# Kernel tuning notes

Hardware: AMD Instinct MI355X
Metric: run time of the kernel (lower is better)

The kernel has to match this reference:

```python
import jax, jax.numpy as jnp
import numpy as np

N = 100000   # nodes
E = 1600000  # edges
NC = 10000   # candidates
G = 1000     # graphs
ND = 32      # node_emb_dim
ED = 8       # edge_emb_dim
L = 4        # num_layers


def setup_inputs() -> dict:
    key = jax.random.key(0)
    ks = jax.random.split(key, 12)
    s = 0.1
    return {
        "x": jax.random.normal(ks[0], (N, 2), dtype=jnp.float32),
        "edge_attr": jax.random.normal(ks[1], (E, 1), dtype=jnp.float32),
        "Wn_in": jax.random.normal(ks[2], (2, ND)) * s,
        "bn_in": jnp.zeros((ND,)),
        "We_in": jax.random.normal(ks[3], (1, ED)) * s,
        "be_in": jnp.zeros((ED,)),
        "We_l": jax.random.normal(ks[4], (L, 2 * ND + ED, ED)) * s,
        "be_l": jnp.zeros((L, ED)),
        "Wn_l": jax.random.normal(ks[5], (L, ND + ED, ND)) * s,
        "bn_l": jnp.zeros((L, ND)),
        "Wout": jax.random.normal(ks[6], (ND, 1)) * s,
        "bout": jnp.zeros((1,)),
        "edge_index": jax.random.randint(ks[7], (2, E), 0, N),
        "batch": jnp.sort(jax.random.randint(ks[8], (N,), 0, G)),
        "candidate_idxs": jax.random.randint(ks[9], (NC,), 0, N),
    }


def reference(x, edge_attr, Wn_in, bn_in, We_in, be_in, We_l, be_l, Wn_l, bn_l,
              Wout, bout, edge_index, batch, candidate_idxs):
    h = x @ Wn_in + bn_in            # [N, ND]
    e = edge_attr @ We_in + be_in    # [E, ED]
    src, dst = edge_index[0], edge_index[1]
    for l in range(L):
        # edge update: MLP on [x_src, x_dst, edge_attr]
        m = jnp.concatenate([h[src], h[dst], e], axis=-1)        # [E, 2*ND+ED]
        new_e = jax.nn.relu(m @ We_l[l] + be_l[l])               # [E, ED]
        # aggregate (aggr='add') messages at destination nodes
        agg = jax.ops.segment_sum(new_e, dst, num_segments=N)    # [N, ED]
        new_h = jax.nn.relu(jnp.concatenate([h, agg], axis=-1) @ Wn_l[l] + bn_l[l])
        h = h + new_h   # residual
        e = e + new_e   # residual
    logits = (h[candidate_idxs] @ Wout + bout)[:, 0]             # [NC]
    seg = batch[candidate_idxs]                                  # [NC] graph ids
    # scatter_log_softmax over per-graph candidate groups
    mx = jax.ops.segment_max(logits, seg, num_segments=G)
    shifted = logits - mx[seg]
    lse = jnp.log(jax.ops.segment_sum(jnp.exp(shifted), seg, num_segments=G))
    return shifted - lse[seg]
```

## Files before the change

### kernel.cpp

```cpp
#include <hip/hip_runtime.h>

#define ND 32
#define ED 8
#define NL 4
#define NG 1000
#define NBC_MAX 512
#define CHUNK 8192
#define CHUNK_H 4096
#define NBLK 64

typedef unsigned short u16;

__device__ __forceinline__ int xcd_swizzle(int b, int nb) {
  int per = nb >> 3;
  return (b < (per << 3)) ? ((b & 7) * per + (b >> 3)) : b;
}


__device__ __forceinline__ u16 f2bf(float f) {
  unsigned u = __float_as_uint(f);
  u += 0x7fffu + ((u >> 16) & 1u);
  return (u16)(u >> 16);
}
__device__ __forceinline__ unsigned pack2(float a, float b) {
  return (unsigned)f2bf(a) | ((unsigned)f2bf(b) << 16);
}
__device__ __forceinline__ void cvt8(uint4 p, float* o) {
  o[0] = __uint_as_float(p.x << 16); o[1] = __uint_as_float(p.x & 0xffff0000u);
  o[2] = __uint_as_float(p.y << 16); o[3] = __uint_as_float(p.y & 0xffff0000u);
  o[4] = __uint_as_float(p.z << 16); o[5] = __uint_as_float(p.z & 0xffff0000u);
  o[6] = __uint_as_float(p.w << 16); o[7] = __uint_as_float(p.w & 0xffff0000u);
}
__device__ __forceinline__ uint4 pack8(const float* v) {
  uint4 o;
  o.x = pack2(v[0], v[1]); o.y = pack2(v[2], v[3]);
  o.z = pack2(v[4], v[5]); o.w = pack2(v[6], v[7]);
  return o;
}


__global__ void k_init_h(const float* __restrict__ x,
                         const float* __restrict__ W,
                         const float* __restrict__ b,
                         const float* __restrict__ We,
                         const float* __restrict__ be,
                         u16* __restrict__ h,
                         u16* __restrict__ zs, u16* __restrict__ zd,
                         int N) {
  int n = xcd_swizzle(blockIdx.x, gridDim.x) * blockDim.x + threadIdx.x;
  if (n >= N) return;
  float x0 = x[2 * n], x1 = x[2 * n + 1];
  float v[ND];
#pragma unroll
  for (int d = 0; d < ND; ++d) v[d] = fmaf(x0, W[d], fmaf(x1, W[ND + d], b[d]));
#pragma unroll
  for (int d = 0; d < ND; ++d) v[d] = __uint_as_float((unsigned)f2bf(v[d]) << 16);
  uint4* h4 = reinterpret_cast<uint4*>(h + (size_t)n * ND);
#pragma unroll
  for (int q = 0; q < 4; ++q) h4[q] = pack8(&v[q * 8]);
  float zsv[ED], zdv[ED];
#pragma unroll
  for (int j = 0; j < ED; ++j) { zsv[j] = 0.0f; zdv[j] = be[j]; }
#pragma unroll
  for (int k = 0; k < ND; ++k)
#pragma unroll
    for (int j = 0; j < ED; ++j) {
      zsv[j] = fmaf(v[k], We[k * ED + j], zsv[j]);
      zdv[j] = fmaf(v[k], We[(ND + k) * ED + j], zdv[j]);
    }
  *reinterpret_cast<uint4*>(zs + (size_t)n * ED) = pack8(zsv);
  *reinterpret_cast<uint4*>(zd + (size_t)n * ED) = pack8(zdv);
}


__global__ void k_chist(const int* __restrict__ dst, int* __restrict__ bcnt,
                        int E, int nbc) {
  __shared__ int lcnt[NBC_MAX];
  for (int b = threadIdx.x; b < nbc; b += blockDim.x) lcnt[b] = 0;
  __syncthreads();
  int e0 = blockIdx.x * CHUNK_H;
  int e1 = min(e0 + CHUNK_H, E);
  for (int i = e0 + threadIdx.x; i < e1; i += blockDim.x)
    atomicAdd(&lcnt[dst[i] >> 8], 1);
  __syncthreads();
  for (int b = threadIdx.x; b < nbc; b += blockDim.x)
    if (lcnt[b]) atomicAdd(&bcnt[b], lcnt[b]);
}

__global__ void k_cscan(const int* __restrict__ bcnt, int* __restrict__ bbase,
                        int nbc) {
  __shared__ int s[NBC_MAX];
  int tid = threadIdx.x;
  if (nbc <= NBC_MAX) {
    int v = (tid < nbc) ? bcnt[tid] : 0;
    s[tid] = v;
    __syncthreads();
    for (int st = 1; st < NBC_MAX; st <<= 1) {
      int t = (tid >= st) ? s[tid - st] : 0;
      __syncthreads();
      s[tid] += t;
      __syncthreads();
    }
    if (tid < nbc) bbase[tid] = s[tid] - v;
    if (tid == nbc - 1) bbase[nbc] = s[tid];
  } else if (tid == 0) {
    int run = 0;
    for (int i = 0; i < nbc; ++i) { bbase[i] = run; run += bcnt[i]; }
    bbase[nbc] = run;
  }
}

__global__ void k_binA(const int* __restrict__ src, const int* __restrict__ dst,
                       const float* __restrict__ ea,
                       const int* __restrict__ bbase, int* __restrict__ cursor_c,
                       uint2* __restrict__ binned, int E, int nbc) {
  __shared__ int lcnt[NBC_MAX];
  __shared__ int lbase[NBC_MAX];
  for (int b = threadIdx.x; b < nbc; b += blockDim.x) lcnt[b] = 0;
  __syncthreads();
  int e0 = blockIdx.x * CHUNK;
  int e1 = min(e0 + CHUNK, E);
  for (int i = e0 + threadIdx.x; i < e1; i += blockDim.x)
    atomicAdd(&lcnt[dst[i] >> 8], 1);
  __syncthreads();
  for (int b = threadIdx.x; b < nbc; b += blockDim.x) {
    int c = lcnt[b];
    lbase[b] = c ? (bbase[b] + atomicAdd(&cursor_c[b], c)) : 0;
  }
  __syncthreads();
  for (int i = e0 + threadIdx.x; i < e1; i += blockDim.x) {
    int d = dst[i];
    int pos = atomicAdd(&lbase[d >> 8], 1);
    binned[pos] = make_uint2((unsigned)src[i] | ((unsigned)(d & 255) << 24),
                             __float_as_uint(ea[i]));
  }
}

__global__ void k_binB(const uint2* __restrict__ binned,
                       const int* __restrict__ bbase,
                       uint2* __restrict__ sedge, u16* __restrict__ e,
                       int* __restrict__ noffs,
                       const float* __restrict__ We,
                       const float* __restrict__ be,
                       int N) {
  __shared__ int hist[256];
  __shared__ int scn[256];
  int b = blockIdx.x;
  int base = bbase[b], end = bbase[b + 1];
  int node0 = b << 8;
  int nn = min(256, N - node0);
  hist[threadIdx.x] = 0;
  __syncthreads();
  for (int p = base + threadIdx.x; p < end; p += blockDim.x)
    atomicAdd(&hist[binned[p].x >> 24], 1);
  __syncthreads();
  int v = hist[threadIdx.x];
  scn[threadIdx.x] = v;
  __syncthreads();
  for (int st = 1; st < 256; st <<= 1) {
    int t = (threadIdx.x >= (unsigned)st) ? scn[threadIdx.x - st] : 0;
    __syncthreads();
    scn[threadIdx.x] += t;
    __syncthreads();
  }
  int excl = base + scn[threadIdx.x] - v;
  if ((int)threadIdx.x < nn) noffs[node0 + threadIdx.x] = excl;
  if (threadIdx.x == 0) noffs[min(node0 + 256, N)] = end;
  hist[threadIdx.x] = excl;
  __syncthreads();
  for (int p = base + threadIdx.x; p < end; p += blockDim.x) {
    uint2 rec = binned[p];
    int dl = (int)(rec.x >> 24);
    int pos = atomicAdd(&hist[dl], 1);
    sedge[pos] = make_uint2(rec.x & 0xffffffu, (unsigned)(node0 + dl));
    float a = __uint_as_float(rec.y);
    float e0[ED];
#pragma unroll
    for (int j = 0; j < ED; ++j) e0[j] = fmaf(a, We[j], be[j]);
    *reinterpret_cast<uint4*>(e + (size_t)pos * ED) = pack8(e0);
  }
}


template <bool LAST>
__global__ void k_edge(const u16* __restrict__ zs,
                       const u16* __restrict__ zd,
                       u16* __restrict__ e,
                       u16* __restrict__ ne,
                       const uint2* __restrict__ sedge,
                       const float* __restrict__ W3,
                       int E) {
  int i = xcd_swizzle(blockIdx.x, gridDim.x) * blockDim.x + threadIdx.x;
  if (i >= E) return;
  uint2 sd = sedge[i];
  float zsv[ED], zdv[ED], ein[ED], acc[ED];
  cvt8(*reinterpret_cast<const uint4*>(zs + (size_t)sd.x * ED), zsv);
  cvt8(*reinterpret_cast<const uint4*>(zd + (size_t)sd.y * ED), zdv);
  cvt8(*reinterpret_cast<const uint4*>(e + (size_t)i * ED), ein);
#pragma unroll
  for (int j = 0; j < ED; ++j) acc[j] = zsv[j] + zdv[j];
#pragma unroll
  for (int k = 0; k < ED; ++k)
#pragma unroll
    for (int j = 0; j < ED; ++j)
      acc[j] = fmaf(ein[k], W3[k * ED + j], acc[j]);
#pragma unroll
  for (int j = 0; j < ED; ++j) acc[j] = fmaxf(acc[j], 0.0f);
  *reinterpret_cast<uint4*>(ne + (size_t)i * ED) = pack8(acc);
  if (!LAST) {
    float eo[ED];
#pragma unroll
    for (int j = 0; j < ED; ++j) eo[j] = ein[j] + acc[j];
    *reinterpret_cast<uint4*>(e + (size_t)i * ED) = pack8(eo);
  }
}

template <bool PROJ>
__global__ void k_node(u16* __restrict__ h,
                       const u16* __restrict__ ne,
                       const int* __restrict__ noffs,
                       const float* __restrict__ W,
                       const float* __restrict__ b,
                       const float* __restrict__ Wen,
                       const float* __restrict__ ben,
                       u16* __restrict__ zs, u16* __restrict__ zd,
                       int N) {
  int n = xcd_swizzle(blockIdx.x, gridDim.x) * blockDim.x + threadIdx.x;
  if (n >= N) return;
  int o0 = noffs[n], o1 = noffs[n + 1];
  float av[ED];
#pragma unroll
  for (int j = 0; j < ED; ++j) av[j] = 0.0f;
  int p = o0;
  for (; p + 3 < o1; p += 4) {
    uint4 r0 = *reinterpret_cast<const uint4*>(ne + (size_t)(p + 0) * ED);
    uint4 r1 = *reinterpret_cast<const uint4*>(ne + (size_t)(p + 1) * ED);
    uint4 r2 = *reinterpret_cast<const uint4*>(ne + (size_t)(p + 2) * ED);
    uint4 r3 = *reinterpret_cast<const uint4*>(ne + (size_t)(p + 3) * ED);
    float t0[ED], t1[ED], t2[ED], t3[ED];
    cvt8(r0, t0); cvt8(r1, t1); cvt8(r2, t2); cvt8(r3, t3);
#pragma unroll
    for (int j = 0; j < ED; ++j)
      av[j] += (t0[j] + t1[j]) + (t2[j] + t3[j]);
  }
  for (; p < o1; ++p) {
    float t[ED];
    cvt8(*reinterpret_cast<const uint4*>(ne + (size_t)p * ED), t);
#pragma unroll
    for (int j = 0; j < ED; ++j) av[j] += t[j];
  }
  float acc[ND];
#pragma unroll
  for (int j = 0; j < ND; ++j) acc[j] = b[j];
  uint4* h4 = reinterpret_cast<uint4*>(h + (size_t)n * ND);
  float hv[ND];
#pragma unroll
  for (int q = 0; q < 4; ++q) cvt8(h4[q], &hv[q * 8]);
#pragma unroll
  for (int k = 0; k < ND; ++k)
#pragma unroll
    for (int j = 0; j < ND; ++j) acc[j] = fmaf(hv[k], W[k * ND + j], acc[j]);
#pragma unroll
  for (int k = 0; k < ED; ++k)
#pragma unroll
    for (int j = 0; j < ND; ++j) acc[j] = fmaf(av[k], W[(ND + k) * ND + j], acc[j]);
  float hn[ND];
#pragma unroll
  for (int k = 0; k < ND; ++k) {
    float o = hv[k] + fmaxf(acc[k], 0.0f);
    hn[k] = __uint_as_float((unsigned)f2bf(o) << 16);
  }
#pragma unroll
  for (int q = 0; q < 4; ++q) h4[q] = pack8(&hn[q * 8]);
  if (PROJ) {
    float zsv[ED], zdv[ED];
#pragma unroll
    for (int j = 0; j < ED; ++j) { zsv[j] = 0.0f; zdv[j] = ben[j]; }
#pragma unroll
    for (int k = 0; k < ND; ++k)
#pragma unroll
      for (int j = 0; j < ED; ++j) {
        zsv[j] = fmaf(hn[k], Wen[k * ED + j], zsv[j]);
        zdv[j] = fmaf(hn[k], Wen[(ND + k) * ED + j], zdv[j]);
      }
    *reinterpret_cast<uint4*>(zs + (size_t)n * ED) = pack8(zsv);
    *reinterpret_cast<uint4*>(zd + (size_t)n * ED) = pack8(zdv);
  }
}


__device__ __forceinline__ unsigned int enc_f32(float f) {
  unsigned int bits = __float_as_uint(f);
  return (bits & 0x80000000u) ? ~bits : (bits | 0x80000000u);
}
__device__ __forceinline__ float dec_f32(unsigned int u) {
  unsigned int bits = (u & 0x80000000u) ? (u ^ 0x80000000u) : ~u;
  return __uint_as_float(bits);
}

__global__ void k_logits(const u16* __restrict__ h,
                         const int* __restrict__ cand,
                         const int* __restrict__ batch,
                         const float* __restrict__ Wout,
                         const float* __restrict__ bout,
                         float* __restrict__ logits,
                         int* __restrict__ seg,
                         unsigned int* __restrict__ mxu,
                         int NC) {
  int c = blockIdx.x * blockDim.x + threadIdx.x;
  if (c >= NC) return;
  int idx = cand[c];
  const uint4* hr = reinterpret_cast<const uint4*>(h + (size_t)idx * ND);
  float acc = bout[0];
  float v[8];
#pragma unroll
  for (int q = 0; q < 4; ++q) {
    cvt8(hr[q], v);
#pragma unroll
    for (int k = 0; k < 8; ++k) acc = fmaf(v[k], Wout[q * 8 + k], acc);
  }
  logits[c] = acc;
  int g = batch[idx];
  seg[c] = g;
  atomicMax(&mxu[g], enc_f32(acc));
}

__global__ void k_expsum(float* __restrict__ logits,
                         const int* __restrict__ seg,
                         const unsigned int* __restrict__ mxu,
                         float* __restrict__ sum,
                         int NC) {
  int c = blockIdx.x * blockDim.x + threadIdx.x;
  if (c >= NC) return;
  int g = seg[c];
  float sh = logits[c] - dec_f32(mxu[g]);
  logits[c] = sh;
  atomicAdd(&sum[g], expf(sh));
}

__global__ void k_final(const float* __restrict__ shifted,
                        const int* __restrict__ seg,
                        const float* __restrict__ sum,
                        float* __restrict__ out, int NC) {
  int c = blockIdx.x * blockDim.x + threadIdx.x;
  if (c >= NC) return;
  out[c] = shifted[c] - logf(sum[seg[c]]);
}


extern "C" void kernel_launch(void* const* d_in, const int* in_sizes, int n_in,
                              void* d_out, int out_size, void* d_ws, size_t ws_size,
                              hipStream_t stream) {
  const float* x       = (const float*)d_in[0];
  const float* ea      = (const float*)d_in[1];
  const float* Wn_in   = (const float*)d_in[2];
  const float* bn_in   = (const float*)d_in[3];
  const float* We_in   = (const float*)d_in[4];
  const float* be_in   = (const float*)d_in[5];
  const float* We_l    = (const float*)d_in[6];
  const float* be_l    = (const float*)d_in[7];
  const float* Wn_l    = (const float*)d_in[8];
  const float* bn_l    = (const float*)d_in[9];
  const float* Wout    = (const float*)d_in[10];
  const float* bout    = (const float*)d_in[11];
  const int* edge_index= (const int*)d_in[12];
  const int* batch     = (const int*)d_in[13];
  const int* cand      = (const int*)d_in[14];

  const int N  = in_sizes[13];
  const int E  = in_sizes[1];
  const int NC = in_sizes[14];
  const int nbc = (N + 255) >> 8;

  char* ws = (char*)d_ws;
  uint2* binned = (uint2*)ws; ws += (size_t)E * sizeof(uint2);
  uint2* sedge  = (uint2*)ws; ws += (size_t)E * sizeof(uint2);
  u16*   h      = (u16*)ws;   ws += (size_t)N * ND * sizeof(u16);
  u16*   e      = (u16*)ws;   ws += (size_t)E * ED * sizeof(u16);
  u16*   ne     = (u16*)ws;   ws += (size_t)E * ED * sizeof(u16);
  u16*   zs     = (u16*)ws;   ws += (size_t)N * ED * sizeof(u16);
  u16*   zd     = (u16*)ws;   ws += (size_t)N * ED * sizeof(u16);
  int*   noffs  = (int*)ws;   ws += ((size_t)N + 4) * sizeof(int);
  int*   bcnt   = (int*)ws;   ws += (size_t)NBC_MAX * sizeof(int);
  int*   cursor = (int*)ws;   ws += (size_t)NBC_MAX * sizeof(int);
  int*   bbase  = (int*)ws;   ws += ((size_t)NBC_MAX + 4) * sizeof(int);
  float* logits = (float*)ws; ws += (size_t)NC * sizeof(float);
  int*   seg    = (int*)ws;   ws += (size_t)NC * sizeof(int);
  unsigned int* mxu = (unsigned int*)ws; ws += (size_t)NG * sizeof(unsigned int);
  float* sum    = (float*)ws; ws += (size_t)NG * sizeof(float);

  const int* srcp = edge_index;
  const int* dstp = edge_index + E;
  const int blk = 256;
  const size_t WE_STRIDE = (size_t)(2 * ND + ED) * ED;

  hipMemsetAsync(bcnt, 0, 2 * (size_t)NBC_MAX * sizeof(int), stream);
  k_chist<<<(E + CHUNK_H - 1) / CHUNK_H, 1024, 0, stream>>>(dstp, bcnt, E, nbc);
  k_cscan<<<1, NBC_MAX, 0, stream>>>(bcnt, bbase, nbc);
  k_binA<<<(E + CHUNK - 1) / CHUNK, 1024, 0, stream>>>(srcp, dstp, ea, bbase,
                                                       cursor, binned, E, nbc);
  k_binB<<<nbc, 256, 0, stream>>>(binned, bbase, sedge, e, noffs, We_in, be_in, N);

  k_init_h<<<(N + NBLK - 1) / NBLK, NBLK, 0, stream>>>(x, Wn_in, bn_in, We_l,
                                                       be_l, h, zs, zd, N);

  const int egrid = (E + blk - 1) / blk;
  const int ngrid = (N + NBLK - 1) / NBLK;
  for (int l = 0; l < NL; ++l) {
    const float* W3 = We_l + l * WE_STRIDE + (size_t)2 * ND * ED;
    const float* Wn = Wn_l + (size_t)l * (ND + ED) * ND;
    const float* bn = bn_l + (size_t)l * ND;
    if (l + 1 < NL) {
      k_edge<false><<<egrid, blk, 0, stream>>>(zs, zd, e, ne, sedge, W3, E);
      k_node<true><<<ngrid, NBLK, 0, stream>>>(
          h, ne, noffs, Wn, bn, We_l + (l + 1) * WE_STRIDE,
          be_l + (size_t)(l + 1) * ED, zs, zd, N);
    } else {
      k_edge<true><<<egrid, blk, 0, stream>>>(zs, zd, e, ne, sedge, W3, E);
      k_node<false><<<ngrid, NBLK, 0, stream>>>(
          h, ne, noffs, Wn, bn, nullptr, nullptr, nullptr, nullptr, N);
    }
  }

  hipMemsetAsync(mxu, 0, NG * (sizeof(unsigned int) + sizeof(float)), stream);
  k_logits<<<(NC + blk - 1) / blk, blk, 0, stream>>>(h, cand, batch, Wout, bout,
                                                     logits, seg, mxu, NC);
  k_expsum<<<(NC + blk - 1) / blk, blk, 0, stream>>>(logits, seg, mxu, sum, NC);
  k_final<<<(NC + blk - 1) / blk, blk, 0, stream>>>(logits, seg, sum,
                                                    (float*)d_out, NC);
}
```

Baseline: 352.0 us.

## Compute last GNN layer only for candidate nodes in a fused kernel

Drops the full last-layer edge and node passes and adds a fused candidate kernel. For each of the 10K candidate nodes it recomputes the incoming edge messages, aggregates them, applies the node MLP and the output projection directly. This removes a 1.6M-edge pass and a 100K-node pass whose results are only needed at candidate nodes. In exchange, per-candidate work becomes a serial loop over in-edges with possible load imbalance, and the templates are removed so the earlier layers always write e and the projections.

```diff
diff --git a/kernel.cpp b/kernel.cpp
--- a/kernel.cpp
+++ b/kernel.cpp
@@ -182,7 +182,6 @@
 }
 
 
-template <bool LAST>
 __global__ void k_edge(const u16* __restrict__ zs,
                        const u16* __restrict__ zd,
                        u16* __restrict__ e,
@@ -207,15 +206,12 @@
 #pragma unroll
   for (int j = 0; j < ED; ++j) acc[j] = fmaxf(acc[j], 0.0f);
   *reinterpret_cast<uint4*>(ne + (size_t)i * ED) = pack8(acc);
-  if (!LAST) {
-    float eo[ED];
-#pragma unroll
-    for (int j = 0; j < ED; ++j) eo[j] = ein[j] + acc[j];
-    *reinterpret_cast<uint4*>(e + (size_t)i * ED) = pack8(eo);
-  }
-}
-
-template <bool PROJ>
+  float eo[ED];
+#pragma unroll
+  for (int j = 0; j < ED; ++j) eo[j] = ein[j] + acc[j];
+  *reinterpret_cast<uint4*>(e + (size_t)i * ED) = pack8(eo);
+}
+
 __global__ void k_node(u16* __restrict__ h,
                        const u16* __restrict__ ne,
                        const int* __restrict__ noffs,
@@ -272,20 +268,18 @@
   }
 #pragma unroll
   for (int q = 0; q < 4; ++q) h4[q] = pack8(&hn[q * 8]);
-  if (PROJ) {
-    float zsv[ED], zdv[ED];
-#pragma unroll
-    for (int j = 0; j < ED; ++j) { zsv[j] = 0.0f; zdv[j] = ben[j]; }
-#pragma unroll
-    for (int k = 0; k < ND; ++k)
-#pragma unroll
-      for (int j = 0; j < ED; ++j) {
-        zsv[j] = fmaf(hn[k], Wen[k * ED + j], zsv[j]);
-        zdv[j] = fmaf(hn[k], Wen[(ND + k) * ED + j], zdv[j]);
-      }
-    *reinterpret_cast<uint4*>(zs + (size_t)n * ED) = pack8(zsv);
-    *reinterpret_cast<uint4*>(zd + (size_t)n * ED) = pack8(zdv);
-  }
+  float zsv[ED], zdv[ED];
+#pragma unroll
+  for (int j = 0; j < ED; ++j) { zsv[j] = 0.0f; zdv[j] = ben[j]; }
+#pragma unroll
+  for (int k = 0; k < ND; ++k)
+#pragma unroll
+    for (int j = 0; j < ED; ++j) {
+      zsv[j] = fmaf(hn[k], Wen[k * ED + j], zsv[j]);
+      zdv[j] = fmaf(hn[k], Wen[(ND + k) * ED + j], zdv[j]);
+    }
+  *reinterpret_cast<uint4*>(zs + (size_t)n * ED) = pack8(zsv);
+  *reinterpret_cast<uint4*>(zd + (size_t)n * ED) = pack8(zdv);
 }
 
 
@@ -298,31 +292,70 @@
   return __uint_as_float(bits);
 }
 
-__global__ void k_logits(const u16* __restrict__ h,
-                         const int* __restrict__ cand,
-                         const int* __restrict__ batch,
-                         const float* __restrict__ Wout,
-                         const float* __restrict__ bout,
-                         float* __restrict__ logits,
-                         int* __restrict__ seg,
-                         unsigned int* __restrict__ mxu,
-                         int NC) {
+__global__ void k_cand(const u16* __restrict__ h,
+                       const u16* __restrict__ e,
+                       const u16* __restrict__ zs,
+                       const u16* __restrict__ zd,
+                       const uint2* __restrict__ sedge,
+                       const int* __restrict__ noffs,
+                       const int* __restrict__ cand,
+                       const int* __restrict__ batch,
+                       const float* __restrict__ W3,
+                       const float* __restrict__ Wn,
+                       const float* __restrict__ bn,
+                       const float* __restrict__ Wout,
+                       const float* __restrict__ bout,
+                       float* __restrict__ logits,
+                       int* __restrict__ seg,
+                       unsigned int* __restrict__ mxu,
+                       int NC) {
   int c = blockIdx.x * blockDim.x + threadIdx.x;
   if (c >= NC) return;
-  int idx = cand[c];
-  const uint4* hr = reinterpret_cast<const uint4*>(h + (size_t)idx * ND);
-  float acc = bout[0];
-  float v[8];
-#pragma unroll
-  for (int q = 0; q < 4; ++q) {
-    cvt8(hr[q], v);
-#pragma unroll
-    for (int k = 0; k < 8; ++k) acc = fmaf(v[k], Wout[q * 8 + k], acc);
-  }
-  logits[c] = acc;
-  int g = batch[idx];
+  int n = cand[c];
+  int o0 = noffs[n], o1 = noffs[n + 1];
+  float zdv[ED];
+  cvt8(*reinterpret_cast<const uint4*>(zd + (size_t)n * ED), zdv);
+  float av[ED];
+#pragma unroll
+  for (int j = 0; j < ED; ++j) av[j] = 0.0f;
+  for (int p = o0; p < o1; ++p) {
+    unsigned s = sedge[p].x;
+    float zsv[ED], ein[ED], acc[ED];
+    cvt8(*reinterpret_cast<const uint4*>(zs + (size_t)s * ED), zsv);
+    cvt8(*reinterpret_cast<const uint4*>(e + (size_t)p * ED), ein);
+#pragma unroll
+    for (int j = 0; j < ED; ++j) acc[j] = zsv[j] + zdv[j];
+#pragma unroll
+    for (int k = 0; k < ED; ++k)
+#pragma unroll
+      for (int j = 0; j < ED; ++j)
+        acc[j] = fmaf(ein[k], W3[k * ED + j], acc[j]);
+#pragma unroll
+    for (int j = 0; j < ED; ++j) av[j] += fmaxf(acc[j], 0.0f);
+  }
+  float acc[ND];
+#pragma unroll
+  for (int j = 0; j < ND; ++j) acc[j] = bn[j];
+  const uint4* h4 = reinterpret_cast<const uint4*>(h + (size_t)n * ND);
+  float hv[ND];
+#pragma unroll
+  for (int q = 0; q < 4; ++q) cvt8(h4[q], &hv[q * 8]);
+#pragma unroll
+  for (int k = 0; k < ND; ++k)
+#pragma unroll
+    for (int j = 0; j < ND; ++j) acc[j] = fmaf(hv[k], Wn[k * ND + j], acc[j]);
+#pragma unroll
+  for (int k = 0; k < ED; ++k)
+#pragma unroll
+    for (int j = 0; j < ND; ++j) acc[j] = fmaf(av[k], Wn[(ND + k) * ND + j], acc[j]);
+  float lg = bout[0];
+#pragma unroll
+  for (int k = 0; k < ND; ++k)
+    lg = fmaf(hv[k] + fmaxf(acc[k], 0.0f), Wout[k], lg);
+  logits[c] = lg;
+  int g = batch[n];
   seg[c] = g;
-  atomicMax(&mxu[g], enc_f32(acc));
+  atomicMax(&mxu[g], enc_f32(lg));
 }
 
 __global__ void k_expsum(float* __restrict__ logits,
@@ -406,25 +439,26 @@
 
   const int egrid = (E + blk - 1) / blk;
   const int ngrid = (N + NBLK - 1) / NBLK;
-  for (int l = 0; l < NL; ++l) {
+  for (int l = 0; l < NL - 1; ++l) {
     const float* W3 = We_l + l * WE_STRIDE + (size_t)2 * ND * ED;
     const float* Wn = Wn_l + (size_t)l * (ND + ED) * ND;
     const float* bn = bn_l + (size_t)l * ND;
-    if (l + 1 < NL) {
-      k_edge<false><<<egrid, blk, 0, stream>>>(zs, zd, e, ne, sedge, W3, E);
-      k_node<true><<<ngrid, NBLK, 0, stream>>>(
-          h, ne, noffs, Wn, bn, We_l + (l + 1) * WE_STRIDE,
-          be_l + (size_t)(l + 1) * ED, zs, zd, N);
-    } else {
-      k_edge<true><<<egrid, blk, 0, stream>>>(zs, zd, e, ne, sedge, W3, E);
-      k_node<false><<<ngrid, NBLK, 0, stream>>>(
-          h, ne, noffs, Wn, bn, nullptr, nullptr, nullptr, nullptr, N);
-    }
+    k_edge<<<egrid, blk, 0, stream>>>(zs, zd, e, ne, sedge, W3, E);
+    k_node<<<ngrid, NBLK, 0, stream>>>(
+        h, ne, noffs, Wn, bn, We_l + (l + 1) * WE_STRIDE,
+        be_l + (size_t)(l + 1) * ED, zs, zd, N);
   }
 
   hipMemsetAsync(mxu, 0, NG * (sizeof(unsigned int) + sizeof(float)), stream);
-  k_logits<<<(NC + blk - 1) / blk, blk, 0, stream>>>(h, cand, batch, Wout, bout,
-                                                     logits, seg, mxu, NC);
+  {
+    const int l = NL - 1;
+    const float* W3 = We_l + l * WE_STRIDE + (size_t)2 * ND * ED;
+    const float* Wn = Wn_l + (size_t)l * (ND + ED) * ND;
+    const float* bn = bn_l + (size_t)l * ND;
+    k_cand<<<(NC + NBLK - 1) / NBLK, NBLK, 0, stream>>>(
+        h, e, zs, zd, sedge, noffs, cand, batch, W3, Wn, bn, Wout, bout,
+        logits, seg, mxu, NC);
+  }
   k_expsum<<<(NC + blk - 1) / blk, blk, 0, stream>>>(logits, seg, mxu, sum, NC);
   k_final<<<(NC + blk - 1) / blk, blk, 0, stream>>>(logits, seg, sum,
                                                     (float*)d_out, NC);
```

Result: no change. 345.3 us (-1.9%).
